# Performance work log

Hardware: AMD Instinct MI355X
Metric: run time of the kernel (lower is better)

## Reference

```python
import jax, jax.numpy as jnp
import numpy as np

DIM = 2048
DIM_HEAD = 64
NUM_HEADS = 32
FFN_INNER = 4 * DIM  # 8192
ATTN_INNER = NUM_HEADS * DIM_HEAD  # 2048
IN_WIDTH = FFN_INNER * 2 + 3 * ATTN_INNER  # 22528
OUT_IN = FFN_INNER + DIM  # 10240
B, S = 1, 2048


def setup_inputs() -> dict:
    key = jax.random.key(0)
    k0, k1, k2 = jax.random.split(key, 3)
    x = jax.random.normal(k0, (B, S, DIM), dtype=jnp.float32)
    W_in = jax.random.normal(k1, (DIM, IN_WIDTH), dtype=jnp.float32) * (DIM ** -0.5)
    W_out = jax.random.normal(k2, (OUT_IN, DIM), dtype=jnp.float32) * (OUT_IN ** -0.5)
    ln_w = jnp.ones((DIM,), dtype=jnp.float32)
    ln_b = jnp.zeros((DIM,), dtype=jnp.float32)
    return {"x": x, "ln_w": ln_w, "ln_b": ln_b, "W_in": W_in, "W_out": W_out}


def _layernorm(x, w, b, eps=1e-5):
    mu = jnp.mean(x, axis=-1, keepdims=True)
    var = jnp.mean(jnp.square(x - mu), axis=-1, keepdims=True)
    return (x - mu) * jax.lax.rsqrt(var + eps) * w + b


def reference(x, ln_w, ln_b, W_in, W_out):
    b, s, _ = x.shape
    h = _layernorm(x, ln_w, ln_b)
    res = h @ W_in  # [b, s, IN_WIDTH]
    q = res[..., :ATTN_INNER]
    k = res[..., ATTN_INNER:2 * ATTN_INNER]
    v = res[..., 2 * ATTN_INNER:3 * ATTN_INNER]
    ffn_input = res[..., 3 * ATTN_INNER:3 * ATTN_INNER + FFN_INNER]
    # b s (h d) -> b h s d
    q = q.reshape(b, s, NUM_HEADS, DIM_HEAD).transpose(0, 2, 1, 3)
    k = k.reshape(b, s, NUM_HEADS, DIM_HEAD).transpose(0, 2, 1, 3)
    v = v.reshape(b, s, NUM_HEADS, DIM_HEAD).transpose(0, 2, 1, 3)
    q = q * (DIM_HEAD ** -0.5)
    sim = jnp.einsum('bhsd,bhnd->bhsn', q, k)  # [b, h, s, s]
    causal = jnp.triu(jnp.ones((s, s), dtype=bool), k=1)
    sim = jnp.where(causal, -jnp.finfo(sim.dtype).max, sim)
    attn = jax.nn.softmax(sim, axis=-1)
    attn_out = jnp.einsum('bhsn,bhnd->bhsd', attn, v)
    attn_out = attn_out.transpose(0, 2, 1, 3).reshape(b, s, ATTN_INNER)
    concat_input = jnp.concatenate([attn_out, ffn_input], axis=-1)  # [b, s, OUT_IN]
    return concat_input @ W_out
```

## Files before the change

kernel.cpp:

```cpp
#include <hip/hip_runtime.h>
#include <stdint.h>

typedef __bf16 bf16x8 __attribute__((ext_vector_type(8)));
typedef float f32x4 __attribute__((ext_vector_type(4)));
typedef uint16_t u16x4 __attribute__((ext_vector_type(4)));
typedef uint16_t u16x8 __attribute__((ext_vector_type(8)));

#define LOG2E 1.4426950408889634f

__device__ __forceinline__ uint16_t f2bf(float f) {
  union { float f; uint32_t u; } v; v.f = f;
  return (uint16_t)((v.u + 0x7fffu + ((v.u >> 16) & 1u)) >> 16);
}

__device__ __forceinline__ void gload_lds16(const void* g, void* l) {
  __builtin_amdgcn_global_load_lds(
      (const __attribute__((address_space(1))) void*)g,
      (__attribute__((address_space(3))) void*)l, 16, 0, 0);
}

__device__ __forceinline__ f32x4 mfma16(bf16x8 a, bf16x8 b, f32x4 c) {
  return __builtin_amdgcn_mfma_f32_16x16x32_bf16(a, b, c, 0, 0, 0);
}

__global__ __launch_bounds__(256) void ln_kernel(const float* __restrict__ x,
                                                 const float* __restrict__ g,
                                                 const float* __restrict__ bta,
                                                 uint16_t* __restrict__ h) {
  const int row = blockIdx.x;
  const int t = threadIdx.x;
  const float* xr = x + (size_t)row * 2048 + t * 8;
  float4 v0 = *(const float4*)xr;
  float4 v1 = *(const float4*)(xr + 4);
  float s = v0.x + v0.y + v0.z + v0.w + v1.x + v1.y + v1.z + v1.w;
  float q = v0.x*v0.x + v0.y*v0.y + v0.z*v0.z + v0.w*v0.w
          + v1.x*v1.x + v1.y*v1.y + v1.z*v1.z + v1.w*v1.w;
  #pragma unroll
  for (int m = 1; m < 64; m <<= 1) {
    s += __shfl_xor(s, m);
    q += __shfl_xor(q, m);
  }
  __shared__ float ps[4], pq[4];
  const int wid = t >> 6, lane = t & 63;
  if (lane == 0) { ps[wid] = s; pq[wid] = q; }
  __syncthreads();
  s = ps[0] + ps[1] + ps[2] + ps[3];
  q = pq[0] + pq[1] + pq[2] + pq[3];
  const float mu = s * (1.0f / 2048.0f);
  const float var = q * (1.0f / 2048.0f) - mu * mu;
  const float rs = rsqrtf(var + 1e-5f);
  float4 w0 = *(const float4*)(g + t * 8);
  float4 w1 = *(const float4*)(g + t * 8 + 4);
  float4 b0 = *(const float4*)(bta + t * 8);
  float4 b1 = *(const float4*)(bta + t * 8 + 4);
  u16x8 o;
  o[0] = f2bf((v0.x - mu) * rs * w0.x + b0.x);
  o[1] = f2bf((v0.y - mu) * rs * w0.y + b0.y);
  o[2] = f2bf((v0.z - mu) * rs * w0.z + b0.z);
  o[3] = f2bf((v0.w - mu) * rs * w0.w + b0.w);
  o[4] = f2bf((v1.x - mu) * rs * w1.x + b1.x);
  o[5] = f2bf((v1.y - mu) * rs * w1.y + b1.y);
  o[6] = f2bf((v1.z - mu) * rs * w1.z + b1.z);
  o[7] = f2bf((v1.w - mu) * rs * w1.w + b1.w);
  *(u16x8*)(h + (size_t)row * 2048 + t * 8) = o;
}

__global__ __launch_bounds__(256) void transpose_w(const float* __restrict__ in,
                                                   uint16_t* __restrict__ out,
                                                   int R, int ldin,
                                                   int scale_cols, float scale) {
  __shared__ uint16_t tile[64][65];
  const int c0 = blockIdx.x * 64;
  const int r0 = blockIdx.y * 64;
  const int t = threadIdx.x;
  const int cc = (t & 15) * 4;
  const int rb = t >> 4;
  #pragma unroll
  for (int p = 0; p < 4; ++p) {
    const int r = rb + p * 16;
    const float4 v = *(const float4*)(in + (size_t)(r0 + r) * ldin + c0 + cc);
    const float m0 = (c0 + cc + 0) < scale_cols ? scale : 1.0f;
    const float m1 = (c0 + cc + 1) < scale_cols ? scale : 1.0f;
    const float m2 = (c0 + cc + 2) < scale_cols ? scale : 1.0f;
    const float m3 = (c0 + cc + 3) < scale_cols ? scale : 1.0f;
    tile[r][cc + 0] = f2bf(v.x * m0);
    tile[r][cc + 1] = f2bf(v.y * m1);
    tile[r][cc + 2] = f2bf(v.z * m2);
    tile[r][cc + 3] = f2bf(v.w * m3);
  }
  __syncthreads();
  #pragma unroll
  for (int p = 0; p < 4; ++p) {
    const int oc = rb + p * 16;
    u16x4 ov;
    ov.x = tile[cc + 0][oc];
    ov.y = tile[cc + 1][oc];
    ov.z = tile[cc + 2][oc];
    ov.w = tile[cc + 3][oc];
    *(u16x4*)(out + (size_t)(c0 + oc) * R + r0 + cc) = ov;
  }
}

__global__ __launch_bounds__(256) void transpose_v(const uint16_t* __restrict__ res,
                                                   uint16_t* __restrict__ vt) {
  __shared__ uint16_t tile[64][65];
  const int c0 = blockIdx.x * 64;
  const int r0 = blockIdx.y * 64;
  const int t = threadIdx.x;
  const int cc = (t & 15) * 4;
  const int rb = t >> 4;
  #pragma unroll
  for (int p = 0; p < 4; ++p) {
    const int r = rb + p * 16;
    const u16x4 v = *(const u16x4*)(res + (size_t)(r0 + r) * 14336 + 4096 + c0 + cc);
    tile[r][cc + 0] = v.x;
    tile[r][cc + 1] = v.y;
    tile[r][cc + 2] = v.z;
    tile[r][cc + 3] = v.w;
  }
  __syncthreads();
  #pragma unroll
  for (int p = 0; p < 4; ++p) {
    const int oc = rb + p * 16;
    u16x4 ov;
    ov.x = tile[cc + 0][oc];
    ov.y = tile[cc + 1][oc];
    ov.z = tile[cc + 2][oc];
    ov.w = tile[cc + 3][oc];
    *(u16x4*)(vt + (size_t)(c0 + oc) * 2048 + r0 + cc) = ov;
  }
}

template <int CONCAT, int CF32>
__global__ __launch_bounds__(512, 2) void gemm_bw(
    const uint16_t* __restrict__ A0, const uint16_t* __restrict__ A1,
    const uint16_t* __restrict__ B, void* __restrict__ C0, void* __restrict__ C1,
    int ldbK, int ldc, int kchunk, int nt) {
  __shared__ __attribute__((aligned(16))) uint16_t Alds[2][128 * 32];
  __shared__ __attribute__((aligned(16))) uint16_t Blds[2][256 * 32];
  const int bid = blockIdx.x;
  const int qx = gridDim.x >> 3;
  const int wg = (bid & 7) * qx + (bid >> 3);
  const int m0 = (wg & 15) << 7;
  const int n0 = (wg >> 4) << 8;
  const int sk = blockIdx.y;
  const int k0 = sk * kchunk;
  const int t = threadIdx.x, wid = t >> 6, lane = t & 63;
  const int wr = wid >> 2, wc = wid & 3;

  f32x4 acc[4][4] = {};

  auto stage = [&](int tt) {
    const int kg = k0 + tt * 32;
    const uint16_t* As; int lda, kc;
    if (CONCAT && kg >= 2048) { As = A1; lda = 14336; kc = kg + 4096; }
    else                      { As = A0; lda = 2048;  kc = kg; }
    char* ab = (char*)Alds[tt & 1];
    char* bb = (char*)Blds[tt & 1];
    {
      const int ch = t;
      const int r = ch >> 2, s = ch & 3;
      gload_lds16(As + (size_t)(m0 + r) * lda + kc + ((s ^ ((r >> 1) & 3)) << 3),
                  ab + ch * 16);
    }
    #pragma unroll
    for (int j = 0; j < 2; ++j) {
      const int ch = j * 512 + t;
      const int r = ch >> 2, s = ch & 3;
      gload_lds16(B + (size_t)(n0 + r) * ldbK + kg + ((s ^ ((r >> 1) & 3)) << 3),
                  bb + ch * 16);
    }
  };

  stage(0);
  for (int tt = 0; tt < nt; ++tt) {
    const int buf = tt & 1;
    asm volatile("s_waitcnt vmcnt(0)" ::: "memory");
    __builtin_amdgcn_s_barrier();
    __builtin_amdgcn_sched_barrier(0);
    if (tt + 1 < nt) stage(tt + 1);
    const char* Ab = (const char*)Alds[buf];
    const char* Bb = (const char*)Blds[buf];
    bf16x8 bfr[4], af[4];
    #pragma unroll
    for (int n = 0; n < 4; ++n) {
      const int r = wc * 64 + n * 16 + (lane & 15);
      const int c = (lane >> 4) ^ ((r >> 1) & 3);
      bfr[n] = *(const bf16x8*)(Bb + r * 64 + c * 16);
    }
    #pragma unroll
    for (int m = 0; m < 4; ++m) {
      const int r = wr * 64 + m * 16 + (lane & 15);
      const int c = (lane >> 4) ^ ((r >> 1) & 3);
      af[m] = *(const bf16x8*)(Ab + r * 64 + c * 16);
    }
    #pragma unroll
    for (int m = 0; m < 4; ++m)
      #pragma unroll
      for (int n = 0; n < 4; ++n)
        acc[m][n] = mfma16(af[m], bfr[n], acc[m][n]);
    __builtin_amdgcn_sched_barrier(0);
  }

  #pragma unroll
  for (int m = 0; m < 4; ++m)
    #pragma unroll
    for (int n = 0; n < 4; ++n)
      #pragma unroll
      for (int r = 0; r < 4; ++r) {
        const int row = m0 + wr * 64 + m * 16 + (lane >> 4) * 4 + r;
        const int col = n0 + wc * 64 + n * 16 + (lane & 15);
        if (CF32) {
          float* C = (sk == 0) ? (float*)C0
                               : ((float*)C1 + (size_t)(sk - 1) * 4194304ull);
          C[(size_t)row * ldc + col] = acc[m][n][r];
        } else {
          ((uint16_t*)C0)[(size_t)row * ldc + col] = f2bf(acc[m][n][r]);
        }
      }
}

__global__ __launch_bounds__(256) void reduce_add3(float* __restrict__ out,
                                                   const float* __restrict__ p) {
  const size_t i = ((size_t)blockIdx.x * 256 + threadIdx.x) * 4;
  float4 a = *(const float4*)(out + i);
  const float4 b = *(const float4*)(p + i);
  const float4 c = *(const float4*)(p + 4194304 + i);
  const float4 d = *(const float4*)(p + 8388608 + i);
  a.x += b.x + c.x + d.x;
  a.y += b.y + c.y + d.y;
  a.z += b.z + c.z + d.z;
  a.w += b.w + c.w + d.w;
  *(float4*)(out + i) = a;
}

__global__ __launch_bounds__(256, 2) void attn_kernel(const uint16_t* __restrict__ res,
                                                      const uint16_t* __restrict__ vt,
                                                      uint16_t* __restrict__ aout) {
  const int hh = blockIdx.y;
  const int qt = (hh < 16) ? blockIdx.x : 15 - blockIdx.x;
  const int q0 = qt * 128;
  const int t = threadIdx.x, wid = t >> 6, lane = t & 63;
  const int qw = q0 + wid * 32;
  __shared__ __attribute__((aligned(16))) uint16_t Klds[3][64 * 64];
  __shared__ __attribute__((aligned(16))) uint16_t Vlds[3][64 * 64];
  __shared__ __attribute__((aligned(16))) uint16_t Plds[4 * 32 * 64];
  char* pbase = (char*)Plds + wid * 4096;

  bf16x8 qf[2][2];
  #pragma unroll
  for (int m = 0; m < 2; ++m)
    #pragma unroll
    for (int ks = 0; ks < 2; ++ks)
      qf[m][ks] = *(const bf16x8*)(res + (size_t)(qw + m * 16 + (lane & 15)) * 14336
                                   + hh * 64 + ks * 32 + (lane >> 4) * 8);
  f32x4 O[2][4] = {};
  f32x4 mrun[2], lrun[2];
  #pragma unroll
  for (int m = 0; m < 2; ++m)
    #pragma unroll
    for (int r = 0; r < 4; ++r) { mrun[m][r] = -1e30f; lrun[m][r] = 0.0f; }

  auto stageKV = [&](int kt) {
    const int k0 = kt * 64;
    char* kb = (char*)Klds[kt % 3];
    char* vb = (char*)Vlds[kt % 3];
    #pragma unroll
    for (int i = 0; i < 2; ++i) {
      const int o = (wid * 2 + i) * 1024 + lane * 16;
      const int row = o >> 7;
      const int slot = (o >> 4) & 7;
      const int col = (slot ^ (row & 7)) << 3;
      gload_lds16(res + (size_t)(k0 + row) * 14336 + 2048 + hh * 64 + col,
                  kb + (wid * 2 + i) * 1024);
      gload_lds16(vt + (size_t)(hh * 64 + row) * 2048 + k0 + col,
                  vb + (wid * 2 + i) * 1024);
    }
  };

  const int nkt = qt * 2 + 2;
  stageKV(0);
  if (1 < nkt) stageKV(1);
  for (int kt = 0; kt < nkt; ++kt) {
    const int k0 = kt * 64;
    if (kt + 1 < nkt) { asm volatile("s_waitcnt vmcnt(4)" ::: "memory"); }
    else              { asm volatile("s_waitcnt vmcnt(0)" ::: "memory"); }
    __builtin_amdgcn_s_barrier();
    __builtin_amdgcn_sched_barrier(0);
    if (kt + 2 < nkt) stageKV(kt + 2);
    if (k0 <= qw + 31) {
      const char* Kb = (const char*)Klds[kt % 3];
      const char* Vb = (const char*)Vlds[kt % 3];
      f32x4 s[2][4] = {};
      #pragma unroll
      for (int ks = 0; ks < 2; ++ks) {
        bf16x8 kf[4];
        #pragma unroll
        for (int n = 0; n < 4; ++n) {
          const int row = n * 16 + (lane & 15);
          const int slot = (ks * 4 + (lane >> 4)) ^ (row & 7);
          kf[n] = *(const bf16x8*)(Kb + row * 128 + slot * 16);
        }
        #pragma unroll
        for (int m = 0; m < 2; ++m)
          #pragma unroll
          for (int n = 0; n < 4; ++n)
            s[m][n] = mfma16(qf[m][ks], kf[n], s[m][n]);
      }
      if (k0 + 63 > qw) {
        #pragma unroll
        for (int m = 0; m < 2; ++m)
          #pragma unroll
          for (int n = 0; n < 4; ++n)
            #pragma unroll
            for (int r = 0; r < 4; ++r) {
              const int key = k0 + n * 16 + (lane & 15);
              const int qr = qw + m * 16 + (lane >> 4) * 4 + r;
              if (key > qr) s[m][n][r] = -1e30f;
            }
      }
      #pragma unroll
      for (int m = 0; m < 2; ++m) {
        f32x4 tmax = s[m][0];
        #pragma unroll
        for (int n = 1; n < 4; ++n)
          #pragma unroll
          for (int r = 0; r < 4; ++r) tmax[r] = fmaxf(tmax[r], s[m][n][r]);
        #pragma unroll
        for (int msk = 1; msk < 16; msk <<= 1)
          #pragma unroll
          for (int r = 0; r < 4; ++r) tmax[r] = fmaxf(tmax[r], __shfl_xor(tmax[r], msk));
        f32x4 newm, sc;
        #pragma unroll
        for (int r = 0; r < 4; ++r) {
          newm[r] = fmaxf(mrun[m][r], tmax[r]);
          sc[r] = exp2f((mrun[m][r] - newm[r]) * LOG2E);
          mrun[m][r] = newm[r];
        }
        f32x4 psum;
        #pragma unroll
        for (int r = 0; r < 4; ++r) psum[r] = 0.0f;
        #pragma unroll
        for (int n = 0; n < 4; ++n)
          #pragma unroll
          for (int r = 0; r < 4; ++r) {
            const float p = exp2f((s[m][n][r] - newm[r]) * LOG2E);
            s[m][n][r] = p;
            psum[r] += p;
          }
        #pragma unroll
        for (int msk = 1; msk < 16; msk <<= 1)
          #pragma unroll
          for (int r = 0; r < 4; ++r) psum[r] += __shfl_xor(psum[r], msk);
        #pragma unroll
        for (int r = 0; r < 4; ++r) lrun[m][r] = lrun[m][r] * sc[r] + psum[r];
        #pragma unroll
        for (int d = 0; d < 4; ++d)
          #pragma unroll
          for (int r = 0; r < 4; ++r) O[m][d][r] *= sc[r];
        #pragma unroll
        for (int n = 0; n < 4; ++n)
          #pragma unroll
          for (int r = 0; r < 4; ++r) {
            const int prow = m * 16 + (lane >> 4) * 4 + r;
            const int pcol = n * 16 + (lane & 15);
            *(uint16_t*)(pbase + prow * 128 + (((pcol >> 3) ^ (prow & 7)) << 4)
                         + (pcol & 7) * 2) = f2bf(s[m][n][r]);
          }
      }
      asm volatile("s_waitcnt lgkmcnt(0)" ::: "memory");
      __builtin_amdgcn_sched_barrier(0);
      #pragma unroll
      for (int ks = 0; ks < 2; ++ks) {
        bf16x8 pa[2], vf[4];
        #pragma unroll
        for (int m = 0; m < 2; ++m) {
          const int row = m * 16 + (lane & 15);
          const int slot = (ks * 4 + (lane >> 4)) ^ (row & 7);
          pa[m] = *(const bf16x8*)(pbase + row * 128 + slot * 16);
        }
        #pragma unroll
        for (int d = 0; d < 4; ++d) {
          const int row = d * 16 + (lane & 15);
          const int slot = (ks * 4 + (lane >> 4)) ^ (row & 7);
          vf[d] = *(const bf16x8*)(Vb + row * 128 + slot * 16);
        }
        #pragma unroll
        for (int m = 0; m < 2; ++m)
          #pragma unroll
          for (int d = 0; d < 4; ++d)
            O[m][d] = mfma16(pa[m], vf[d], O[m][d]);
      }
    }
  }
  #pragma unroll
  for (int m = 0; m < 2; ++m) {
    f32x4 inv;
    #pragma unroll
    for (int r = 0; r < 4; ++r) inv[r] = 1.0f / lrun[m][r];
    #pragma unroll
    for (int d = 0; d < 4; ++d)
      #pragma unroll
      for (int r = 0; r < 4; ++r) {
        const int row = qw + m * 16 + (lane >> 4) * 4 + r;
        const int col = hh * 64 + d * 16 + (lane & 15);
        aout[(size_t)row * 2048 + col] = f2bf(O[m][d][r] * inv[r]);
      }
  }
}

extern "C" void kernel_launch(void* const* d_in, const int* in_sizes, int n_in,
                              void* d_out, int out_size, void* d_ws, size_t ws_size,
                              hipStream_t stream) {
  (void)in_sizes; (void)n_in; (void)out_size;
  const float* x     = (const float*)d_in[0];
  const float* ln_w  = (const float*)d_in[1];
  const float* ln_b  = (const float*)d_in[2];
  const float* W_in  = (const float*)d_in[3];
  const float* W_out = (const float*)d_in[4];

  const size_t need = 184549376ull;
  if (ws_size < need) return;
  char* ws = (char*)d_ws;
  size_t off = 0;
  uint16_t* h     = (uint16_t*)(ws + off); off += (size_t)2048 * 2048 * 2;
  uint16_t* WtIn  = (uint16_t*)(ws + off); off += (size_t)14336 * 2048 * 2;
  uint16_t* WtOut = (uint16_t*)(ws + off); off += (size_t)2048 * 10240 * 2;
  uint16_t* res   = (uint16_t*)(ws + off); off += (size_t)2048 * 14336 * 2;
  uint16_t* vt    = (uint16_t*)(ws + off); off += (size_t)2048 * 2048 * 2;
  uint16_t* aout  = (uint16_t*)(ws + off);
  float* partials = (float*)ws;

  ln_kernel<<<2048, 256, 0, stream>>>(x, ln_w, ln_b, h);
  transpose_w<<<dim3(224, 32), 256, 0, stream>>>(W_in, WtIn, 2048, 22528, 2048, 0.125f);
  transpose_w<<<dim3(32, 160), 256, 0, stream>>>(W_out, WtOut, 10240, 2048, 0, 1.0f);
  gemm_bw<0, 0><<<dim3(896, 1), 512, 0, stream>>>(h, nullptr, WtIn, res, nullptr,
                                                  2048, 14336, 0, 64);
  transpose_v<<<dim3(32, 32), 256, 0, stream>>>(res, vt);
  attn_kernel<<<dim3(16, 32), 256, 0, stream>>>(res, vt, aout);
  gemm_bw<1, 1><<<dim3(128, 4), 512, 0, stream>>>(aout, res, WtOut, d_out, partials,
                                                  10240, 2048, 2560, 80);
  reduce_add3<<<4096, 256, 0, stream>>>((float*)d_out, partials);
}
```

Measured before the change: 406.8 us.

## Fold W_out transpose into QKV GEMM tail blocks and use atomic split-K

The W_out fp32-to-bf16 transpose moves out of its own launch and into 512 extra blocks appended to the first GEMM grid, so it runs alongside the GEMM tiles instead of as a separate kernel. The output GEMM's split-K partials are now accumulated with float atomicAdd into a zeroed output, which removes the partial buffers and the reduce_add3 kernel. In exchange the first GEMM carries extra LDS for the transpose tile, adds a memset launch, and makes the final sum order nondeterministic under atomic contention.

```diff
diff --git a/kernel.cpp b/kernel.cpp
--- a/kernel.cpp
+++ b/kernel.cpp
@@ -131,15 +131,51 @@
   }
 }
 
-template <int CONCAT, int CF32>
-__global__ __launch_bounds__(512, 2) void gemm_bw(
+template <int CONCAT, int ATOM, int TWTAIL>
+__global__ __launch_bounds__(512, 2) void gemm_f(
     const uint16_t* __restrict__ A0, const uint16_t* __restrict__ A1,
-    const uint16_t* __restrict__ B, void* __restrict__ C0, void* __restrict__ C1,
-    int ldbK, int ldc, int kchunk, int nt) {
+    const uint16_t* __restrict__ B, void* __restrict__ C0,
+    const float* __restrict__ Wo, uint16_t* __restrict__ WtOut,
+    int nGemm, int ldbK, int ldc, int kchunk, int nt) {
   __shared__ __attribute__((aligned(16))) uint16_t Alds[2][128 * 32];
   __shared__ __attribute__((aligned(16))) uint16_t Blds[2][256 * 32];
+  __shared__ uint16_t ttile[TWTAIL ? 64 : 1][TWTAIL ? 65 : 1];
+
+  if (TWTAIL && (int)blockIdx.x >= nGemm) {
+    const int nTw = gridDim.x - nGemm;
+    const int t = threadIdx.x;
+    const int cc = (t & 15) * 4;
+    const int rb = t >> 4;
+    for (int tile = (int)blockIdx.x - nGemm; tile < 5120; tile += nTw) {
+      const int c0 = (tile & 31) * 64;
+      const int r0 = (tile >> 5) * 64;
+      #pragma unroll
+      for (int p = 0; p < 2; ++p) {
+        const int r = rb + p * 32;
+        const float4 v = *(const float4*)(Wo + (size_t)(r0 + r) * 2048 + c0 + cc);
+        ttile[r][cc + 0] = f2bf(v.x);
+        ttile[r][cc + 1] = f2bf(v.y);
+        ttile[r][cc + 2] = f2bf(v.z);
+        ttile[r][cc + 3] = f2bf(v.w);
+      }
+      __syncthreads();
+      #pragma unroll
+      for (int p = 0; p < 2; ++p) {
+        const int oc = rb + p * 32;
+        u16x4 ov;
+        ov.x = ttile[cc + 0][oc];
+        ov.y = ttile[cc + 1][oc];
+        ov.z = ttile[cc + 2][oc];
+        ov.w = ttile[cc + 3][oc];
+        *(u16x4*)(WtOut + (size_t)(c0 + oc) * 10240 + r0 + cc) = ov;
+      }
+      __syncthreads();
+    }
+    return;
+  }
+
   const int bid = blockIdx.x;
-  const int qx = gridDim.x >> 3;
+  const int qx = nGemm >> 3;
   const int wg = (bid & 7) * qx + (bid >> 3);
   const int m0 = (wg & 15) << 7;
   const int n0 = (wg >> 4) << 8;
@@ -210,28 +246,12 @@
       for (int r = 0; r < 4; ++r) {
         const int row = m0 + wr * 64 + m * 16 + (lane >> 4) * 4 + r;
         const int col = n0 + wc * 64 + n * 16 + (lane & 15);
-        if (CF32) {
-          float* C = (sk == 0) ? (float*)C0
-                               : ((float*)C1 + (size_t)(sk - 1) * 4194304ull);
-          C[(size_t)row * ldc + col] = acc[m][n][r];
+        if (ATOM) {
+          atomicAdd((float*)C0 + (size_t)row * ldc + col, acc[m][n][r]);
         } else {
           ((uint16_t*)C0)[(size_t)row * ldc + col] = f2bf(acc[m][n][r]);
         }
       }
-}
-
-__global__ __launch_bounds__(256) void reduce_add3(float* __restrict__ out,
-                                                   const float* __restrict__ p) {
-  const size_t i = ((size_t)blockIdx.x * 256 + threadIdx.x) * 4;
-  float4 a = *(const float4*)(out + i);
-  const float4 b = *(const float4*)(p + i);
-  const float4 c = *(const float4*)(p + 4194304 + i);
-  const float4 d = *(const float4*)(p + 8388608 + i);
-  a.x += b.x + c.x + d.x;
-  a.y += b.y + c.y + d.y;
-  a.z += b.z + c.z + d.z;
-  a.w += b.w + c.w + d.w;
-  *(float4*)(out + i) = a;
 }
 
 __global__ __launch_bounds__(256, 2) void attn_kernel(const uint16_t* __restrict__ res,
@@ -429,16 +449,14 @@
   uint16_t* res   = (uint16_t*)(ws + off); off += (size_t)2048 * 14336 * 2;
   uint16_t* vt    = (uint16_t*)(ws + off); off += (size_t)2048 * 2048 * 2;
   uint16_t* aout  = (uint16_t*)(ws + off);
-  float* partials = (float*)ws;
 
   ln_kernel<<<2048, 256, 0, stream>>>(x, ln_w, ln_b, h);
   transpose_w<<<dim3(224, 32), 256, 0, stream>>>(W_in, WtIn, 2048, 22528, 2048, 0.125f);
-  transpose_w<<<dim3(32, 160), 256, 0, stream>>>(W_out, WtOut, 10240, 2048, 0, 1.0f);
-  gemm_bw<0, 0><<<dim3(896, 1), 512, 0, stream>>>(h, nullptr, WtIn, res, nullptr,
-                                                  2048, 14336, 0, 64);
+  gemm_f<0, 0, 1><<<dim3(896 + 512, 1), 512, 0, stream>>>(
+      h, nullptr, WtIn, res, W_out, WtOut, 896, 2048, 14336, 0, 64);
   transpose_v<<<dim3(32, 32), 256, 0, stream>>>(res, vt);
   attn_kernel<<<dim3(16, 32), 256, 0, stream>>>(res, vt, aout);
-  gemm_bw<1, 1><<<dim3(128, 4), 512, 0, stream>>>(aout, res, WtOut, d_out, partials,
-                                                  10240, 2048, 2560, 80);
-  reduce_add3<<<4096, 256, 0, stream>>>((float*)d_out, partials);
-}
+  hipMemsetAsync(d_out, 0, (size_t)2048 * 2048 * 4, stream);
+  gemm_f<1, 1, 0><<<dim3(128, 4), 512, 0, stream>>>(
+      aout, res, WtOut, d_out, nullptr, nullptr, 128, 10240, 2048, 2560, 80);
+}
```

After: 427.9 us. +5.2%, slower.

## Use 256x256 tile GEMM kernel for the input projection

Applied to the files above, without the earlier changes.

Adds a new GEMM kernel with 256x256 output tiles, where each wave computes a 64x128 sub-tile using 4x8 MFMA accumulators. It replaces the 128x256-tile kernel for the large input projection and halves the grid to 448 blocks. The aim is higher arithmetic intensity, with fewer LDS and global loads per MFMA. In exchange it uses more registers and LDS per block (64KB), which may lower occupancy below two blocks per CU, and the grid is smaller.

```diff
diff --git a/kernel.cpp b/kernel.cpp
--- a/kernel.cpp
+++ b/kernel.cpp
@@ -131,6 +131,83 @@
   }
 }
 
+__global__ __launch_bounds__(512, 2) void gemm_sq(
+    const uint16_t* __restrict__ A, const uint16_t* __restrict__ B,
+    uint16_t* __restrict__ C, int ldbK, int ldc, int nt) {
+  __shared__ __attribute__((aligned(16))) uint16_t Alds[2][256 * 32];
+  __shared__ __attribute__((aligned(16))) uint16_t Blds[2][256 * 32];
+  const int bid = blockIdx.x;
+  const int qx = gridDim.x >> 3;
+  const int wg = (bid & 7) * qx + (bid >> 3);
+  const int m0 = (wg & 7) << 8;
+  const int n0 = (wg >> 3) << 8;
+  const int t = threadIdx.x, wid = t >> 6, lane = t & 63;
+  const int wr = wid >> 1, wc = wid & 1;
+
+  f32x4 acc[4][8] = {};
+
+  auto stage = [&](int tt) {
+    const int kg = tt * 32;
+    char* ab = (char*)Alds[tt & 1];
+    char* bb = (char*)Blds[tt & 1];
+    #pragma unroll
+    for (int j = 0; j < 2; ++j) {
+      const int ch = j * 512 + t;
+      const int r = ch >> 2, s = ch & 3;
+      gload_lds16(A + (size_t)(m0 + r) * 2048 + kg + ((s ^ ((r >> 1) & 3)) << 3),
+                  ab + ch * 16);
+    }
+    #pragma unroll
+    for (int j = 0; j < 2; ++j) {
+      const int ch = j * 512 + t;
+      const int r = ch >> 2, s = ch & 3;
+      gload_lds16(B + (size_t)(n0 + r) * ldbK + kg + ((s ^ ((r >> 1) & 3)) << 3),
+                  bb + ch * 16);
+    }
+  };
+
+  stage(0);
+  for (int tt = 0; tt < nt; ++tt) {
+    const int buf = tt & 1;
+    asm volatile("s_waitcnt vmcnt(0)" ::: "memory");
+    __builtin_amdgcn_s_barrier();
+    __builtin_amdgcn_sched_barrier(0);
+    if (tt + 1 < nt) stage(tt + 1);
+    const char* Ab = (const char*)Alds[buf];
+    const char* Bb = (const char*)Blds[buf];
+    bf16x8 bfr[8], af[4];
+    #pragma unroll
+    for (int n = 0; n < 8; ++n) {
+      const int r = wc * 128 + n * 16 + (lane & 15);
+      const int c = (lane >> 4) ^ ((r >> 1) & 3);
+      bfr[n] = *(const bf16x8*)(Bb + r * 64 + c * 16);
+    }
+    #pragma unroll
+    for (int m = 0; m < 4; ++m) {
+      const int r = wr * 64 + m * 16 + (lane & 15);
+      const int c = (lane >> 4) ^ ((r >> 1) & 3);
+      af[m] = *(const bf16x8*)(Ab + r * 64 + c * 16);
+    }
+    #pragma unroll
+    for (int m = 0; m < 4; ++m)
+      #pragma unroll
+      for (int n = 0; n < 8; ++n)
+        acc[m][n] = mfma16(af[m], bfr[n], acc[m][n]);
+    __builtin_amdgcn_sched_barrier(0);
+  }
+
+  #pragma unroll
+  for (int m = 0; m < 4; ++m)
+    #pragma unroll
+    for (int n = 0; n < 8; ++n)
+      #pragma unroll
+      for (int r = 0; r < 4; ++r) {
+        const int row = m0 + wr * 64 + m * 16 + (lane >> 4) * 4 + r;
+        const int col = n0 + wc * 128 + n * 16 + (lane & 15);
+        C[(size_t)row * ldc + col] = f2bf(acc[m][n][r]);
+      }
+}
+
 template <int CONCAT, int CF32>
 __global__ __launch_bounds__(512, 2) void gemm_bw(
     const uint16_t* __restrict__ A0, const uint16_t* __restrict__ A1,
@@ -434,8 +511,7 @@
   ln_kernel<<<2048, 256, 0, stream>>>(x, ln_w, ln_b, h);
   transpose_w<<<dim3(224, 32), 256, 0, stream>>>(W_in, WtIn, 2048, 22528, 2048, 0.125f);
   transpose_w<<<dim3(32, 160), 256, 0, stream>>>(W_out, WtOut, 10240, 2048, 0, 1.0f);
-  gemm_bw<0, 0><<<dim3(896, 1), 512, 0, stream>>>(h, nullptr, WtIn, res, nullptr,
-                                                  2048, 14336, 0, 64);
+  gemm_sq<<<dim3(448, 1), 512, 0, stream>>>(h, WtIn, res, 2048, 14336, 64);
   transpose_v<<<dim3(32, 32), 256, 0, stream>>>(res, vt);
   attn_kernel<<<dim3(16, 32), 256, 0, stream>>>(res, vt, aout);
   gemm_bw<1, 1><<<dim3(128, 4), 512, 0, stream>>>(aout, res, WtOut, d_out, partials,
```

After: 436.8 us. +7.4%, slower.
